# Kernel optimization log

Hardware: AMD Instinct MI355X
Metric: run time of the kernel (lower is better)

The kernel has to match this reference:

```python
import jax, jax.numpy as jnp
import numpy as np

LN_EPS = 1e-5


def _layer_norm(x, g, b):
    m = jnp.mean(x, axis=-1, keepdims=True)
    v = jnp.mean(jnp.square(x - m), axis=-1, keepdims=True)
    return (x - m) * jax.lax.rsqrt(v + LN_EPS) * g + b


def _transition(x, g, bln, w_sw, w_ss, w_sig, b_sig, w_scale, residual):
    # TransitionBlock, eval mode (dropout = identity)
    x_in = x
    x = _layer_norm(x, g, bln)
    b = jax.nn.silu(x @ w_sw.T) * (x @ w_ss.T)
    y = jax.nn.sigmoid(x @ w_sig.T + b_sig) * (b @ w_scale.T)
    return x_in + y if residual else y


def setup_inputs() -> dict:
    N, E = 1000000, 100000
    F_DIM, A_DIM, H_DIM, HEADS = 64, 128, 256, 4
    D_IN = F_DIM + A_DIM
    key = jax.random.key(0)
    ks = jax.random.split(key, 16)
    s = 0.02
    inp = {
        'v_equivariant': jax.random.normal(ks[0], (N, 3), jnp.float32),
        'v_atom_features': jax.random.normal(ks[1], (N, A_DIM), jnp.float32),
        'edge_group_idx': jnp.sort(jax.random.randint(ks[2], (N,), 0, E)).astype(jnp.int32),
        'num_edges': E,
        'fourier_w': jax.random.normal(ks[3], (F_DIM,), jnp.float32),
        'fourier_b': jax.random.normal(ks[4], (F_DIM,), jnp.float32),
        # TransitionBlock 1 (input 192 -> 256, no residual)
        'tb1_ln_g': jnp.ones((D_IN,), jnp.float32),
        'tb1_ln_b': jnp.zeros((D_IN,), jnp.float32),
        'tb1_w_sw': jax.random.normal(ks[5], (H_DIM, D_IN), jnp.float32) * s,
        'tb1_w_ss': jax.random.normal(ks[6], (H_DIM, D_IN), jnp.float32) * s,
        'tb1_w_sig': jax.random.normal(ks[7], (H_DIM, D_IN), jnp.float32) * s,
        'tb1_b_sig': jnp.full((H_DIM,), -2.0, jnp.float32),
        'tb1_w_scale': jax.random.normal(ks[8], (H_DIM, H_DIM), jnp.float32) * s,
        # TransitionBlock 2 (256 -> 256, residual)
        'tb2_ln_g': jnp.ones((H_DIM,), jnp.float32),
        'tb2_ln_b': jnp.zeros((H_DIM,), jnp.float32),
        'tb2_w_sw': jax.random.normal(ks[9], (H_DIM, H_DIM), jnp.float32) * s,
        'tb2_w_ss': jax.random.normal(ks[10], (H_DIM, H_DIM), jnp.float32) * s,
        'tb2_w_sig': jax.random.normal(ks[11], (H_DIM, H_DIM), jnp.float32) * s,
        'tb2_b_sig': jnp.full((H_DIM,), -2.0, jnp.float32),
        'tb2_w_scale': jax.random.normal(ks[12], (H_DIM, H_DIM), jnp.float32) * s,
        # final linear 256 -> num_heads
        'out_w': jax.random.normal(ks[13], (HEADS, H_DIM), jnp.float32) * s,
        'out_b': jnp.zeros((HEADS,), jnp.float32),
    }
    return inp


def reference(v_equivariant, v_atom_features, edge_group_idx, num_edges,
              fourier_w, fourier_b,
              tb1_ln_g, tb1_ln_b, tb1_w_sw, tb1_w_ss, tb1_w_sig, tb1_b_sig, tb1_w_scale,
              tb2_ln_g, tb2_ln_b, tb2_w_sw, tb2_w_ss, tb2_w_sig, tb2_b_sig, tb2_w_scale,
              out_w, out_b):
    # Fourier embedding of vector norms: [N] -> [N, F_DIM]
    v_norms = jnp.linalg.norm(v_equivariant, axis=-1)
    f_dist = jnp.cos(2.0 * jnp.pi * (v_norms[..., None] * fourier_w + fourier_b))
    x = jnp.concatenate([f_dist, v_atom_features], axis=-1)  # [N, 192]
    x = _transition(x, tb1_ln_g, tb1_ln_b, tb1_w_sw, tb1_w_ss, tb1_w_sig, tb1_b_sig, tb1_w_scale, residual=False)
    x = _transition(x, tb2_ln_g, tb2_ln_b, tb2_w_sw, tb2_w_ss, tb2_w_sig, tb2_b_sig, tb2_w_scale, residual=True)
    scores = x @ out_w.T + out_b  # [N, H]
    # scatter_softmax over edge groups (per head)
    smax = jax.ops.segment_max(scores, edge_group_idx, num_segments=num_edges)
    e = jnp.exp(scores - smax[edge_group_idx])
    ssum = jax.ops.segment_sum(e, edge_group_idx, num_segments=num_edges)
    alphas = e / ssum[edge_group_idx]  # [N, H]
    # weighted scatter-sum pooling of 3-vectors per head
    v_weighted = v_equivariant[:, None, :] * alphas[..., None]  # [N, H, 3]
    v_pooled = jax.ops.segment_sum(v_weighted, edge_group_idx, num_segments=num_edges)
    return v_pooled.reshape(num_edges, -1)  # [E, H*3]
```

## Files before the change

### kernel.cpp

```cpp
#include <hip/hip_runtime.h>
#include <math.h>

#define DIN   192
#define HD    256
#define ROWS  64
#define THREADS 512
#define LSTR  256

typedef __bf16 bf16_t;
typedef bf16_t bf16x8 __attribute__((ext_vector_type(8)));
typedef float  f32x16 __attribute__((ext_vector_type(16)));

static __device__ __forceinline__ f32x16 mfma32(bf16x8 a, bf16x8 b, f32x16 c) {
  return __builtin_amdgcn_mfma_f32_32x32x16_bf16(a, b, c, 0, 0, 0);
}
static __device__ __forceinline__ unsigned short f2bfu(float f) {
  bf16_t h = (bf16_t)f; unsigned short u; __builtin_memcpy(&u, &h, 2); return u;
}
static __device__ __forceinline__ float bfu2f(unsigned short u) {
  unsigned x = ((unsigned)u) << 16; float f; __builtin_memcpy(&f, &x, 4); return f;
}
static __device__ __forceinline__ unsigned pk2(float a, float b) {
  return (unsigned)f2bfu(a) | ((unsigned)f2bfu(b) << 16);
}
static __device__ __forceinline__ float lo16(unsigned u) { return bfu2f((unsigned short)(u & 0xffff)); }
static __device__ __forceinline__ float hi16(unsigned u) { return bfu2f((unsigned short)(u >> 16)); }
static __device__ __forceinline__ float sigm(float x) {
  return __builtin_amdgcn_rcpf(1.f + __expf(-x));
}
static __device__ __forceinline__ int lidx(int row, int col) {
  return row * LSTR + (col ^ ((row & 7) << 3));
}
static __device__ __forceinline__ int crow(int r, int kg) {
  return (r & 3) + 8 * (r >> 2) + 4 * kg;
}

#define OFF_WSW1 0
#define OFF_WSS1 49152
#define OFF_WSG1 98304
#define OFF_WSC1 147456
#define OFF_WSW2 212992
#define OFF_WSS2 278528
#define OFF_WSG2 344064
#define OFF_WSC2 409600
#define OFF_WOUT 475136
#define NGRP_REORD 59392
#define NGRP_ALL   60416

__global__ void iab_wconv_kernel(const float* __restrict__ a0, const float* __restrict__ a1,
                                 const float* __restrict__ a2, const float* __restrict__ a3,
                                 const float* __restrict__ a4, const float* __restrict__ a5,
                                 const float* __restrict__ a6, const float* __restrict__ a7,
                                 const float* __restrict__ a8, unsigned short* __restrict__ out)
{
  const int i = blockIdx.x * 256 + threadIdx.x;
  if (i >= NGRP_ALL) return;
  if (i >= NGRP_REORD) {
    const int g  = i - NGRP_REORD;
    const int ks = g >> 6;
    const int ln = g & 63;
    const int col = ln & 31;
    const int kg  = ln >> 5;
    #pragma unroll
    for (int j = 0; j < 8; ++j) {
      const float vv = (col < 4) ? a8[col * 256 + ks * 16 + kg * 8 + j] : 0.f;
      out[OFF_WOUT + (size_t)g * 8 + j] = f2bfu(vv);
    }
    return;
  }
  const float* src; int off, Kd, g;
  if      (i < 6144)  { src = a0; off = OFF_WSW1; Kd = 192; g = i; }
  else if (i < 12288) { src = a1; off = OFF_WSS1; Kd = 192; g = i - 6144; }
  else if (i < 18432) { src = a2; off = OFF_WSG1; Kd = 192; g = i - 12288; }
  else if (i < 26624) { src = a3; off = OFF_WSC1; Kd = 256; g = i - 18432; }
  else if (i < 34816) { src = a4; off = OFF_WSW2; Kd = 256; g = i - 26624; }
  else if (i < 43008) { src = a5; off = OFF_WSS2; Kd = 256; g = i - 34816; }
  else if (i < 51200) { src = a6; off = OFF_WSG2; Kd = 256; g = i - 43008; }
  else                { src = a7; off = OFF_WSC2; Kd = 256; g = i - 51200; }
  const int KS   = Kd >> 4;
  const int tile = g / (KS * 64);
  const int rem  = g - tile * (KS * 64);
  const int ks   = rem >> 6;
  const int ln   = rem & 63;
  const float* sp = src + (size_t)(tile * 32 + (ln & 31)) * Kd + ks * 16 + (ln >> 5) * 8;
  #pragma unroll
  for (int j = 0; j < 8; ++j) out[off + (size_t)g * 8 + j] = f2bfu(sp[j]);
}

template<int KS>
static __device__ __forceinline__ void gemm2(const unsigned short* __restrict__ Wt,
                                             const unsigned short* __restrict__ sIn,
                                             int l31, int kg, int xr,
                                             f32x16& acc0, f32x16& acc1)
{
  #pragma unroll 4
  for (int ks = 0; ks < KS; ++ks) {
    const bf16x8 Wc = *(const bf16x8*)(Wt + ks * 512);
    const int col = (ks * 16 + kg * 8) ^ xr;
    const bf16x8 A0 = *(const bf16x8*)(sIn + l31 * LSTR + col);
    const bf16x8 A1 = *(const bf16x8*)(sIn + (l31 + 32) * LSTR + col);
    acc0 = mfma32(A0, Wc, acc0);
    acc1 = mfma32(A1, Wc, acc1);
  }
}

template<int KS>
static __device__ __forceinline__ void gemm2p(const unsigned short* __restrict__ Wa,
                                              const unsigned short* __restrict__ Wb,
                                              const unsigned short* __restrict__ sIn,
                                              int l31, int kg, int xr,
                                              f32x16& u0, f32x16& u1,
                                              f32x16& s0, f32x16& s1)
{
  #pragma unroll 2
  for (int ks = 0; ks < KS; ++ks) {
    const bf16x8 wa = *(const bf16x8*)(Wa + ks * 512);
    const bf16x8 wb = *(const bf16x8*)(Wb + ks * 512);
    const int col = (ks * 16 + kg * 8) ^ xr;
    const bf16x8 A0 = *(const bf16x8*)(sIn + l31 * LSTR + col);
    const bf16x8 A1 = *(const bf16x8*)(sIn + (l31 + 32) * LSTR + col);
    u0 = mfma32(A0, wa, u0);
    s0 = mfma32(A0, wb, s0);
    u1 = mfma32(A1, wa, u1);
    s1 = mfma32(A1, wb, s1);
  }
}

static __device__ __forceinline__ void storeSilu2(unsigned short* dst, const f32x16 u,
                                                  const f32x16 s, int mt, int kg, int ocol)
{
  #pragma unroll
  for (int i = 0; i < 16; ++i) {
    const float x = u[i];
    dst[lidx(mt * 32 + crow(i, kg), ocol)] = f2bfu(x * sigm(x) * s[i]);
  }
}

static __device__ __forceinline__ void storePk(unsigned short* dst, const unsigned* xp,
                                               int kg, int ocol)
{
  #pragma unroll
  for (int mt = 0; mt < 2; ++mt) {
    #pragma unroll
    for (int p = 0; p < 8; ++p) {
      const int r0 = 2 * p;
      const int row0 = mt * 32 + crow(r0, kg);
      const unsigned pk = xp[mt * 8 + p];
      dst[lidx(row0,     ocol)] = (unsigned short)(pk & 0xffff);
      dst[lidx(row0 + 1, ocol)] = (unsigned short)(pk >> 16);
    }
  }
}

__global__ __launch_bounds__(THREADS, 2)
void iab_rows_mfma(
    const float* __restrict__ v, const float* __restrict__ af,
    const float* __restrict__ fw, const float* __restrict__ fb,
    const float* __restrict__ ln1g, const float* __restrict__ ln1b,
    const float* __restrict__ bsig1,
    const float* __restrict__ ln2g, const float* __restrict__ ln2b,
    const float* __restrict__ bsig2,
    const float* __restrict__ outb,
    const unsigned short* __restrict__ wc,
    float* __restrict__ scores, int N)
{
  __shared__ __align__(16) unsigned short sA[ROWS * LSTR];
  __shared__ __align__(16) unsigned short sB[ROWS * LSTR];

  const int t    = threadIdx.x;
  const int w    = t >> 6;
  const int lane = t & 63;
  const int l31  = lane & 31;
  const int kg   = lane >> 5;
  const int xr   = (lane & 7) << 3;
  const int ocol = w * 32 + l31;
  const int row0 = blockIdx.x * ROWS;

  const unsigned short* WtSW1 = wc + OFF_WSW1 + (w * 12 * 64 + lane) * 8;
  const unsigned short* WtSS1 = wc + OFF_WSS1 + (w * 12 * 64 + lane) * 8;
  const unsigned short* WtSG1 = wc + OFF_WSG1 + (w * 12 * 64 + lane) * 8;
  const unsigned short* WtSC1 = wc + OFF_WSC1 + (w * 16 * 64 + lane) * 8;
  const unsigned short* WtSW2 = wc + OFF_WSW2 + (w * 16 * 64 + lane) * 8;
  const unsigned short* WtSS2 = wc + OFF_WSS2 + (w * 16 * 64 + lane) * 8;
  const unsigned short* WtSG2 = wc + OFF_WSG2 + (w * 16 * 64 + lane) * 8;
  const unsigned short* WtSC2 = wc + OFF_WSC2 + (w * 16 * 64 + lane) * 8;

  {
    const float fwl = fw[lane], fbl = fb[lane];
    const float g1a = ln1g[lane], g1b = ln1g[lane + 64], g1c = ln1g[lane + 128];
    const float o1a = ln1b[lane], o1b = ln1b[lane + 64], o1c = ln1b[lane + 128];
    for (int rr = 0; rr < 8; ++rr) {
      const int r = w * 8 + rr;
      const int g = row0 + r;
      float e0 = 0.f, e1 = 0.f, e2 = 0.f;
      if (g < N) {
        const float vx = v[3 * (size_t)g + 0];
        const float vy = v[3 * (size_t)g + 1];
        const float vz = v[3 * (size_t)g + 2];
        const float nrm = sqrtf(vx * vx + vy * vy + vz * vz);
        e0 = __cosf(6.283185307179586f * (nrm * fwl + fbl));
        const float* a = af + (size_t)g * 128;
        e1 = a[lane];
        e2 = a[lane + 64];
      }
      float s  = e0 + e1 + e2;
      float sq = e0 * e0 + e1 * e1 + e2 * e2;
      #pragma unroll
      for (int o = 32; o >= 1; o >>= 1) {
        s  += __shfl_xor(s,  o);
        sq += __shfl_xor(sq, o);
      }
      const float mean = s * (1.f / 192.f);
      const float var  = fmaxf(sq * (1.f / 192.f) - mean * mean, 0.f);
      const float rstd = rsqrtf(var + 1e-5f);
      sA[lidx(r, lane)]       = f2bfu((e0 - mean) * rstd * g1a + o1a);
      sA[lidx(r, lane + 64)]  = f2bfu((e1 - mean) * rstd * g1b + o1b);
      sA[lidx(r, lane + 128)] = f2bfu((e2 - mean) * rstd * g1c + o1c);
    }
  }
  __syncthreads();

  unsigned x2p[16];

  {
    f32x16 u0{}, u1{}, s0{}, s1{};
    gemm2p<12>(WtSW1, WtSS1, sA, l31, kg, xr, u0, u1, s0, s1);
    storeSilu2(sB, u0, s0, 0, kg, ocol);
    storeSilu2(sB, u1, s1, 1, kg, ocol);
  }

  unsigned sgp[16];
  {
    f32x16 g0{}, g1{};
    gemm2<12>(WtSG1, sA, l31, kg, xr, g0, g1);
    const float bias = bsig1[ocol];
    #pragma unroll
    for (int p = 0; p < 8; ++p) {
      sgp[p]     = pk2(sigm(g0[2*p] + bias), sigm(g0[2*p+1] + bias));
      sgp[8 + p] = pk2(sigm(g1[2*p] + bias), sigm(g1[2*p+1] + bias));
    }
  }
  __syncthreads();

  {
    f32x16 c0{}, c1{};
    gemm2<16>(WtSC1, sB, l31, kg, xr, c0, c1);
    #pragma unroll
    for (int p = 0; p < 8; ++p) {
      x2p[p]     = pk2(lo16(sgp[p])   * c0[2*p], hi16(sgp[p])   * c0[2*p+1]);
      x2p[8 + p] = pk2(lo16(sgp[8+p]) * c1[2*p], hi16(sgp[8+p]) * c1[2*p+1]);
    }
    storePk(sA, x2p, kg, ocol);
  }
  __syncthreads();

  {
    float g2v[4], o2v[4];
    #pragma unroll
    for (int i = 0; i < 4; ++i) { g2v[i] = ln2g[lane + 64 * i]; o2v[i] = ln2b[lane + 64 * i]; }
    for (int rr = 0; rr < 8; ++rr) {
      const int r = w * 8 + rr;
      float e[4];
      #pragma unroll
      for (int i = 0; i < 4; ++i) e[i] = bfu2f(sA[lidx(r, lane + 64 * i)]);
      float s  = e[0] + e[1] + e[2] + e[3];
      float sq = e[0]*e[0] + e[1]*e[1] + e[2]*e[2] + e[3]*e[3];
      #pragma unroll
      for (int o = 32; o >= 1; o >>= 1) {
        s  += __shfl_xor(s,  o);
        sq += __shfl_xor(sq, o);
      }
      const float mean = s * (1.f / 256.f);
      const float var  = fmaxf(sq * (1.f / 256.f) - mean * mean, 0.f);
      const float rstd = rsqrtf(var + 1e-5f);
      #pragma unroll
      for (int i = 0; i < 4; ++i)
        sA[lidx(r, lane + 64 * i)] = f2bfu((e[i] - mean) * rstd * g2v[i] + o2v[i]);
    }
  }
  __syncthreads();

  {
    f32x16 u0{}, u1{}, s0{}, s1{};
    gemm2p<16>(WtSW2, WtSS2, sA, l31, kg, xr, u0, u1, s0, s1);
    storeSilu2(sB, u0, s0, 0, kg, ocol);
    storeSilu2(sB, u1, s1, 1, kg, ocol);
  }

  {
    f32x16 g0{}, g1{};
    gemm2<16>(WtSG2, sA, l31, kg, xr, g0, g1);
    const float bias = bsig2[ocol];
    #pragma unroll
    for (int p = 0; p < 8; ++p) {
      sgp[p]     = pk2(sigm(g0[2*p] + bias), sigm(g0[2*p+1] + bias));
      sgp[8 + p] = pk2(sigm(g1[2*p] + bias), sigm(g1[2*p+1] + bias));
    }
  }
  __syncthreads();

  {
    f32x16 c0{}, c1{};
    gemm2<16>(WtSC2, sB, l31, kg, xr, c0, c1);
    #pragma unroll
    for (int p = 0; p < 8; ++p) {
      x2p[p]     = pk2(lo16(x2p[p])   + lo16(sgp[p])   * c0[2*p],
                       hi16(x2p[p])   + hi16(sgp[p])   * c0[2*p+1]);
      x2p[8 + p] = pk2(lo16(x2p[8+p]) + lo16(sgp[8+p]) * c1[2*p],
                       hi16(x2p[8+p]) + hi16(sgp[8+p]) * c1[2*p+1]);
    }
    storePk(sA, x2p, kg, ocol);
  }
  __syncthreads();

  if (w < 2) {
    const unsigned short* WtF = wc + OFF_WOUT + (size_t)lane * 8;
    f32x16 c{};
    #pragma unroll 4
    for (int ks = 0; ks < 16; ++ks) {
      const bf16x8 wf = *(const bf16x8*)(WtF + ks * 512);
      const int col = (ks * 16 + kg * 8) ^ xr;
      const bf16x8 A = *(const bf16x8*)(sA + (w * 32 + l31) * LSTR + col);
      c = mfma32(A, wf, c);
    }
    if (l31 < 4) {
      const float bias = outb[l31];
      #pragma unroll
      for (int i = 0; i < 16; ++i) {
        const int g = row0 + w * 32 + crow(i, kg);
        if (g < N) scores[(size_t)g * 4 + l31] = c[i] + bias;
      }
    }
  }
}

__device__ __forceinline__ int iab_lower_bound(const int* __restrict__ a, int n, int key)
{
  int lo = 0, hi = n;
  while (lo < hi) {
    const int mid = (lo + hi) >> 1;
    if (a[mid] < key) lo = mid + 1; else hi = mid;
  }
  return lo;
}

__global__ __launch_bounds__(256)
void iab_segpool_kernel(const float* __restrict__ scores,
                        const float* __restrict__ v,
                        const int* __restrict__ gidx,
                        float* __restrict__ out, int N, int E)
{
  const int seg  = blockIdx.x * 4 + (threadIdx.x >> 6);
  const int lane = threadIdx.x & 63;
  if (seg >= E) return;

  const int lo = iab_lower_bound(gidx, N, seg);
  const int hi = iab_lower_bound(gidx, N, seg + 1);

  const int h  = lane & 3;
  const int ro = lane >> 2;

  float m = -INFINITY;
  for (int base = lo; base < hi; base += 16) {
    const int r = base + ro;
    if (r < hi) m = fmaxf(m, scores[(size_t)r * 4 + h]);
  }
  #pragma unroll
  for (int o = 4; o < 64; o <<= 1) m = fmaxf(m, __shfl_xor(m, o));

  float ssum = 0.f, w0 = 0.f, w1 = 0.f, w2 = 0.f;
  for (int base = lo; base < hi; base += 16) {
    const int r = base + ro;
    if (r < hi) {
      const float e = expf(scores[(size_t)r * 4 + h] - m);
      ssum += e;
      w0 += e * v[3 * (size_t)r + 0];
      w1 += e * v[3 * (size_t)r + 1];
      w2 += e * v[3 * (size_t)r + 2];
    }
  }
  #pragma unroll
  for (int o = 4; o < 64; o <<= 1) {
    ssum += __shfl_xor(ssum, o);
    w0   += __shfl_xor(w0, o);
    w1   += __shfl_xor(w1, o);
    w2   += __shfl_xor(w2, o);
  }

  if (ro == 0) {
    const float inv = (hi > lo) ? (1.f / ssum) : 0.f;
    out[(size_t)seg * 12 + h * 3 + 0] = w0 * inv;
    out[(size_t)seg * 12 + h * 3 + 1] = w1 * inv;
    out[(size_t)seg * 12 + h * 3 + 2] = w2 * inv;
  }
}

extern "C" void kernel_launch(void* const* d_in, const int* in_sizes, int n_in,
                              void* d_out, int out_size, void* d_ws, size_t ws_size,
                              hipStream_t stream)
{
  const float* v     = (const float*)d_in[0];
  const float* af    = (const float*)d_in[1];
  const int*   gidx  = (const int*)  d_in[2];
  const float* fw    = (const float*)d_in[4];
  const float* fb    = (const float*)d_in[5];
  const float* ln1g  = (const float*)d_in[6];
  const float* ln1b  = (const float*)d_in[7];
  const float* wsw1  = (const float*)d_in[8];
  const float* wss1  = (const float*)d_in[9];
  const float* wsig1 = (const float*)d_in[10];
  const float* bsig1 = (const float*)d_in[11];
  const float* wsc1  = (const float*)d_in[12];
  const float* ln2g  = (const float*)d_in[13];
  const float* ln2b  = (const float*)d_in[14];
  const float* wsw2  = (const float*)d_in[15];
  const float* wss2  = (const float*)d_in[16];
  const float* wsig2 = (const float*)d_in[17];
  const float* bsig2 = (const float*)d_in[18];
  const float* wsc2  = (const float*)d_in[19];
  const float* outw  = (const float*)d_in[20];
  const float* outb  = (const float*)d_in[21];

  const int N = in_sizes[0] / 3;
  const int E = out_size / 12;

  float* scores = (float*)d_ws;
  unsigned short* wcv = (unsigned short*)((char*)d_ws + (size_t)N * 4 * sizeof(float));

  hipLaunchKernelGGL(iab_wconv_kernel, dim3((NGRP_ALL + 255) / 256), dim3(256), 0, stream,
                     wsw1, wss1, wsig1, wsc1, wsw2, wss2, wsig2, wsc2, outw, wcv);

  hipLaunchKernelGGL(iab_rows_mfma, dim3((N + ROWS - 1) / ROWS), dim3(THREADS), 0, stream,
                     v, af, fw, fb, ln1g, ln1b, bsig1, ln2g, ln2b, bsig2, outb,
                     wcv, scores, N);

  hipLaunchKernelGGL(iab_segpool_kernel, dim3((E + 3) / 4), dim3(256), 0, stream,
                     scores, v, gidx, (float*)d_out, N, E);
}
```

Measured before the change: 1.948 ms.

## Halve row tile to 32 rows with 4 waves each covering two column tiles

The fused MLP kernel now processes 32 rows per block with 256 threads instead of 64 rows with 512 threads. Each wave computes two 32-column output tiles over a single 32-row tile rather than one column tile over two row tiles. Shared memory per block halves and the occupancy hint rises to 5 blocks per SM. The layer norms are rewritten so 8 threads share a row and use vectorized 16-byte LDS and global accesses. The cost is that each weight fragment is reused across only 32 rows, so weight traffic from global or L2 per row doubles.

```diff
diff --git a/kernel.cpp b/kernel.cpp
--- a/kernel.cpp
+++ b/kernel.cpp
@@ -3,12 +3,13 @@
 
 #define DIN   192
 #define HD    256
-#define ROWS  64
-#define THREADS 512
+#define ROWS  32
+#define THREADS 256
 #define LSTR  256
 
 typedef __bf16 bf16_t;
 typedef bf16_t bf16x8 __attribute__((ext_vector_type(8)));
+typedef unsigned short u16x8 __attribute__((ext_vector_type(8)));
 typedef float  f32x16 __attribute__((ext_vector_type(16)));
 
 static __device__ __forceinline__ f32x16 mfma32(bf16x8 a, bf16x8 b, f32x16 c) {
@@ -88,71 +89,58 @@
 }
 
 template<int KS>
-static __device__ __forceinline__ void gemm2(const unsigned short* __restrict__ Wt,
+static __device__ __forceinline__ void gemm1(const unsigned short* __restrict__ Wt,
                                              const unsigned short* __restrict__ sIn,
-                                             int l31, int kg, int xr,
-                                             f32x16& acc0, f32x16& acc1)
+                                             int l31, int kg, int xr, f32x16& acc)
 {
   #pragma unroll 4
   for (int ks = 0; ks < KS; ++ks) {
     const bf16x8 Wc = *(const bf16x8*)(Wt + ks * 512);
-    const int col = (ks * 16 + kg * 8) ^ xr;
-    const bf16x8 A0 = *(const bf16x8*)(sIn + l31 * LSTR + col);
-    const bf16x8 A1 = *(const bf16x8*)(sIn + (l31 + 32) * LSTR + col);
-    acc0 = mfma32(A0, Wc, acc0);
-    acc1 = mfma32(A1, Wc, acc1);
+    const bf16x8 A  = *(const bf16x8*)(sIn + l31 * LSTR + (((ks * 16) + kg * 8) ^ xr));
+    acc = mfma32(A, Wc, acc);
   }
 }
 
 template<int KS>
-static __device__ __forceinline__ void gemm2p(const unsigned short* __restrict__ Wa,
+static __device__ __forceinline__ void gemm1p(const unsigned short* __restrict__ Wa,
                                               const unsigned short* __restrict__ Wb,
                                               const unsigned short* __restrict__ sIn,
                                               int l31, int kg, int xr,
-                                              f32x16& u0, f32x16& u1,
-                                              f32x16& s0, f32x16& s1)
-{
-  #pragma unroll 2
+                                              f32x16& u, f32x16& s)
+{
+  #pragma unroll 4
   for (int ks = 0; ks < KS; ++ks) {
     const bf16x8 wa = *(const bf16x8*)(Wa + ks * 512);
     const bf16x8 wb = *(const bf16x8*)(Wb + ks * 512);
-    const int col = (ks * 16 + kg * 8) ^ xr;
-    const bf16x8 A0 = *(const bf16x8*)(sIn + l31 * LSTR + col);
-    const bf16x8 A1 = *(const bf16x8*)(sIn + (l31 + 32) * LSTR + col);
-    u0 = mfma32(A0, wa, u0);
-    s0 = mfma32(A0, wb, s0);
-    u1 = mfma32(A1, wa, u1);
-    s1 = mfma32(A1, wb, s1);
-  }
-}
-
-static __device__ __forceinline__ void storeSilu2(unsigned short* dst, const f32x16 u,
-                                                  const f32x16 s, int mt, int kg, int ocol)
+    const bf16x8 A  = *(const bf16x8*)(sIn + l31 * LSTR + (((ks * 16) + kg * 8) ^ xr));
+    u = mfma32(A, wa, u);
+    s = mfma32(A, wb, s);
+  }
+}
+
+static __device__ __forceinline__ void storeSilu1(unsigned short* dst, const f32x16 u,
+                                                  const f32x16 s, int kg, int ocol)
 {
   #pragma unroll
   for (int i = 0; i < 16; ++i) {
     const float x = u[i];
-    dst[lidx(mt * 32 + crow(i, kg), ocol)] = f2bfu(x * sigm(x) * s[i]);
-  }
-}
-
-static __device__ __forceinline__ void storePk(unsigned short* dst, const unsigned* xp,
-                                               int kg, int ocol)
-{
-  #pragma unroll
-  for (int mt = 0; mt < 2; ++mt) {
-    #pragma unroll
-    for (int p = 0; p < 8; ++p) {
-      const int r0 = 2 * p;
-      const int row0 = mt * 32 + crow(r0, kg);
-      const unsigned pk = xp[mt * 8 + p];
-      dst[lidx(row0,     ocol)] = (unsigned short)(pk & 0xffff);
-      dst[lidx(row0 + 1, ocol)] = (unsigned short)(pk >> 16);
-    }
-  }
-}
-
-__global__ __launch_bounds__(THREADS, 2)
+    dst[lidx(crow(i, kg), ocol)] = f2bfu(x * sigm(x) * s[i]);
+  }
+}
+
+static __device__ __forceinline__ void storePk1(unsigned short* dst, const unsigned* xp,
+                                                int kg, int ocol)
+{
+  #pragma unroll
+  for (int p = 0; p < 8; ++p) {
+    const int row0 = crow(2 * p, kg);
+    const unsigned pk = xp[p];
+    dst[lidx(row0,     ocol)] = (unsigned short)(pk & 0xffff);
+    dst[lidx(row0 + 1, ocol)] = (unsigned short)(pk >> 16);
+  }
+}
+
+__global__ __launch_bounds__(THREADS, 5)
 void iab_rows_mfma(
     const float* __restrict__ v, const float* __restrict__ af,
     const float* __restrict__ fw, const float* __restrict__ fb,
@@ -173,161 +161,220 @@
   const int l31  = lane & 31;
   const int kg   = lane >> 5;
   const int xr   = (lane & 7) << 3;
-  const int ocol = w * 32 + l31;
   const int row0 = blockIdx.x * ROWS;
 
-  const unsigned short* WtSW1 = wc + OFF_WSW1 + (w * 12 * 64 + lane) * 8;
-  const unsigned short* WtSS1 = wc + OFF_WSS1 + (w * 12 * 64 + lane) * 8;
-  const unsigned short* WtSG1 = wc + OFF_WSG1 + (w * 12 * 64 + lane) * 8;
-  const unsigned short* WtSC1 = wc + OFF_WSC1 + (w * 16 * 64 + lane) * 8;
-  const unsigned short* WtSW2 = wc + OFF_WSW2 + (w * 16 * 64 + lane) * 8;
-  const unsigned short* WtSS2 = wc + OFF_WSS2 + (w * 16 * 64 + lane) * 8;
-  const unsigned short* WtSG2 = wc + OFF_WSG2 + (w * 16 * 64 + lane) * 8;
-  const unsigned short* WtSC2 = wc + OFF_WSC2 + (w * 16 * 64 + lane) * 8;
-
   {
-    const float fwl = fw[lane], fbl = fb[lane];
-    const float g1a = ln1g[lane], g1b = ln1g[lane + 64], g1c = ln1g[lane + 128];
-    const float o1a = ln1b[lane], o1b = ln1b[lane + 64], o1c = ln1b[lane + 128];
-    for (int rr = 0; rr < 8; ++rr) {
-      const int r = w * 8 + rr;
-      const int g = row0 + r;
-      float e0 = 0.f, e1 = 0.f, e2 = 0.f;
-      if (g < N) {
-        const float vx = v[3 * (size_t)g + 0];
-        const float vy = v[3 * (size_t)g + 1];
-        const float vz = v[3 * (size_t)g + 2];
-        const float nrm = sqrtf(vx * vx + vy * vy + vz * vz);
-        e0 = __cosf(6.283185307179586f * (nrm * fwl + fbl));
-        const float* a = af + (size_t)g * 128;
-        e1 = a[lane];
-        e2 = a[lane + 64];
-      }
-      float s  = e0 + e1 + e2;
-      float sq = e0 * e0 + e1 * e1 + e2 * e2;
+    const int r   = t >> 3;
+    const int sub = t & 7;
+    const int g   = row0 + r;
+    const int xrr = (r & 7) << 3;
+    float vx = 0.f, vy = 0.f, vz = 0.f;
+    if (g < N) {
+      vx = v[3 * (size_t)g + 0];
+      vy = v[3 * (size_t)g + 1];
+      vz = v[3 * (size_t)g + 2];
+    }
+    const float nrm = sqrtf(vx * vx + vy * vy + vz * vz);
+    float e[24];
+    {
+      const float4 fwa = *(const float4*)(fw + sub * 8);
+      const float4 fwb = *(const float4*)(fw + sub * 8 + 4);
+      const float4 fba = *(const float4*)(fb + sub * 8);
+      const float4 fbb = *(const float4*)(fb + sub * 8 + 4);
+      e[0] = __cosf(6.283185307179586f * (nrm * fwa.x + fba.x));
+      e[1] = __cosf(6.283185307179586f * (nrm * fwa.y + fba.y));
+      e[2] = __cosf(6.283185307179586f * (nrm * fwa.z + fba.z));
+      e[3] = __cosf(6.283185307179586f * (nrm * fwa.w + fba.w));
+      e[4] = __cosf(6.283185307179586f * (nrm * fwb.x + fbb.x));
+      e[5] = __cosf(6.283185307179586f * (nrm * fwb.y + fbb.y));
+      e[6] = __cosf(6.283185307179586f * (nrm * fwb.z + fbb.z));
+      e[7] = __cosf(6.283185307179586f * (nrm * fwb.w + fbb.w));
+    }
+    if (g < N) {
+      const float* ap = af + (size_t)g * 128 + sub * 8;
+      const float4 a0 = *(const float4*)(ap);
+      const float4 a1 = *(const float4*)(ap + 4);
+      const float4 a2 = *(const float4*)(ap + 64);
+      const float4 a3 = *(const float4*)(ap + 68);
+      e[8]  = a0.x; e[9]  = a0.y; e[10] = a0.z; e[11] = a0.w;
+      e[12] = a1.x; e[13] = a1.y; e[14] = a1.z; e[15] = a1.w;
+      e[16] = a2.x; e[17] = a2.y; e[18] = a2.z; e[19] = a2.w;
+      e[20] = a3.x; e[21] = a3.y; e[22] = a3.z; e[23] = a3.w;
+    } else {
       #pragma unroll
-      for (int o = 32; o >= 1; o >>= 1) {
-        s  += __shfl_xor(s,  o);
-        sq += __shfl_xor(sq, o);
-      }
-      const float mean = s * (1.f / 192.f);
-      const float var  = fmaxf(sq * (1.f / 192.f) - mean * mean, 0.f);
-      const float rstd = rsqrtf(var + 1e-5f);
-      sA[lidx(r, lane)]       = f2bfu((e0 - mean) * rstd * g1a + o1a);
-      sA[lidx(r, lane + 64)]  = f2bfu((e1 - mean) * rstd * g1b + o1b);
-      sA[lidx(r, lane + 128)] = f2bfu((e2 - mean) * rstd * g1c + o1c);
+      for (int j = 8; j < 24; ++j) e[j] = 0.f;
+    }
+    float s = 0.f, sq = 0.f;
+    #pragma unroll
+    for (int j = 0; j < 24; ++j) { s += e[j]; sq += e[j] * e[j]; }
+    #pragma unroll
+    for (int o = 1; o < 8; o <<= 1) {
+      s  += __shfl_xor(s,  o);
+      sq += __shfl_xor(sq, o);
+    }
+    const float mean = s * (1.f / 192.f);
+    const float var  = fmaxf(sq * (1.f / 192.f) - mean * mean, 0.f);
+    const float rstd = rsqrtf(var + 1e-5f);
+    #pragma unroll
+    for (int ch = 0; ch < 3; ++ch) {
+      const int base = ch * 64 + sub * 8;
+      const float4 ga = *(const float4*)(ln1g + base);
+      const float4 gb = *(const float4*)(ln1g + base + 4);
+      const float4 oa = *(const float4*)(ln1b + base);
+      const float4 ob = *(const float4*)(ln1b + base + 4);
+      u16x8 p;
+      p[0] = f2bfu((e[ch*8+0] - mean) * rstd * ga.x + oa.x);
+      p[1] = f2bfu((e[ch*8+1] - mean) * rstd * ga.y + oa.y);
+      p[2] = f2bfu((e[ch*8+2] - mean) * rstd * ga.z + oa.z);
+      p[3] = f2bfu((e[ch*8+3] - mean) * rstd * ga.w + oa.w);
+      p[4] = f2bfu((e[ch*8+4] - mean) * rstd * gb.x + ob.x);
+      p[5] = f2bfu((e[ch*8+5] - mean) * rstd * gb.y + ob.y);
+      p[6] = f2bfu((e[ch*8+6] - mean) * rstd * gb.z + ob.z);
+      p[7] = f2bfu((e[ch*8+7] - mean) * rstd * gb.w + ob.w);
+      *(u16x8*)(sA + r * LSTR + (base ^ xrr)) = p;
     }
   }
   __syncthreads();
 
   unsigned x2p[16];
+  unsigned sgp[16];
+
+  #pragma unroll
+  for (int c = 0; c < 2; ++c) {
+    const int ocol = w * 64 + c * 32 + l31;
+    const int T = w * 2 + c;
+    f32x16 u{}, s{};
+    gemm1p<12>(wc + OFF_WSW1 + T * 12 * 512 + lane * 8,
+               wc + OFF_WSS1 + T * 12 * 512 + lane * 8, sA, l31, kg, xr, u, s);
+    storeSilu1(sB, u, s, kg, ocol);
+  }
+
+  #pragma unroll
+  for (int c = 0; c < 2; ++c) {
+    const int ocol = w * 64 + c * 32 + l31;
+    const int T = w * 2 + c;
+    f32x16 gacc{};
+    gemm1<12>(wc + OFF_WSG1 + T * 12 * 512 + lane * 8, sA, l31, kg, xr, gacc);
+    const float bias = bsig1[ocol];
+    #pragma unroll
+    for (int p = 0; p < 8; ++p)
+      sgp[c * 8 + p] = pk2(sigm(gacc[2*p] + bias), sigm(gacc[2*p+1] + bias));
+  }
+  __syncthreads();
+
+  #pragma unroll
+  for (int c = 0; c < 2; ++c) {
+    const int ocol = w * 64 + c * 32 + l31;
+    const int T = w * 2 + c;
+    f32x16 cacc{};
+    gemm1<16>(wc + OFF_WSC1 + T * 16 * 512 + lane * 8, sB, l31, kg, xr, cacc);
+    #pragma unroll
+    for (int p = 0; p < 8; ++p)
+      x2p[c * 8 + p] = pk2(lo16(sgp[c*8+p]) * cacc[2*p],
+                           hi16(sgp[c*8+p]) * cacc[2*p+1]);
+    storePk1(sA, x2p + c * 8, kg, ocol);
+  }
+  __syncthreads();
 
   {
-    f32x16 u0{}, u1{}, s0{}, s1{};
-    gemm2p<12>(WtSW1, WtSS1, sA, l31, kg, xr, u0, u1, s0, s1);
-    storeSilu2(sB, u0, s0, 0, kg, ocol);
-    storeSilu2(sB, u1, s1, 1, kg, ocol);
-  }
-
-  unsigned sgp[16];
-  {
-    f32x16 g0{}, g1{};
-    gemm2<12>(WtSG1, sA, l31, kg, xr, g0, g1);
-    const float bias = bsig1[ocol];
-    #pragma unroll
-    for (int p = 0; p < 8; ++p) {
-      sgp[p]     = pk2(sigm(g0[2*p] + bias), sigm(g0[2*p+1] + bias));
-      sgp[8 + p] = pk2(sigm(g1[2*p] + bias), sigm(g1[2*p+1] + bias));
-    }
-  }
-  __syncthreads();
-
-  {
-    f32x16 c0{}, c1{};
-    gemm2<16>(WtSC1, sB, l31, kg, xr, c0, c1);
-    #pragma unroll
-    for (int p = 0; p < 8; ++p) {
-      x2p[p]     = pk2(lo16(sgp[p])   * c0[2*p], hi16(sgp[p])   * c0[2*p+1]);
-      x2p[8 + p] = pk2(lo16(sgp[8+p]) * c1[2*p], hi16(sgp[8+p]) * c1[2*p+1]);
-    }
-    storePk(sA, x2p, kg, ocol);
-  }
-  __syncthreads();
-
-  {
-    float g2v[4], o2v[4];
-    #pragma unroll
-    for (int i = 0; i < 4; ++i) { g2v[i] = ln2g[lane + 64 * i]; o2v[i] = ln2b[lane + 64 * i]; }
-    for (int rr = 0; rr < 8; ++rr) {
-      const int r = w * 8 + rr;
-      float e[4];
-      #pragma unroll
-      for (int i = 0; i < 4; ++i) e[i] = bfu2f(sA[lidx(r, lane + 64 * i)]);
-      float s  = e[0] + e[1] + e[2] + e[3];
-      float sq = e[0]*e[0] + e[1]*e[1] + e[2]*e[2] + e[3]*e[3];
-      #pragma unroll
-      for (int o = 32; o >= 1; o >>= 1) {
-        s  += __shfl_xor(s,  o);
-        sq += __shfl_xor(sq, o);
-      }
-      const float mean = s * (1.f / 256.f);
-      const float var  = fmaxf(sq * (1.f / 256.f) - mean * mean, 0.f);
-      const float rstd = rsqrtf(var + 1e-5f);
-      #pragma unroll
-      for (int i = 0; i < 4; ++i)
-        sA[lidx(r, lane + 64 * i)] = f2bfu((e[i] - mean) * rstd * g2v[i] + o2v[i]);
-    }
-  }
-  __syncthreads();
-
-  {
-    f32x16 u0{}, u1{}, s0{}, s1{};
-    gemm2p<16>(WtSW2, WtSS2, sA, l31, kg, xr, u0, u1, s0, s1);
-    storeSilu2(sB, u0, s0, 0, kg, ocol);
-    storeSilu2(sB, u1, s1, 1, kg, ocol);
-  }
-
-  {
-    f32x16 g0{}, g1{};
-    gemm2<16>(WtSG2, sA, l31, kg, xr, g0, g1);
+    const int r   = t >> 3;
+    const int sub = t & 7;
+    const int xrr = (r & 7) << 3;
+    u16x8 rv0 = *(const u16x8*)(sA + r * LSTR + ((sub * 32 +  0) ^ xrr));
+    u16x8 rv1 = *(const u16x8*)(sA + r * LSTR + ((sub * 32 +  8) ^ xrr));
+    u16x8 rv2 = *(const u16x8*)(sA + r * LSTR + ((sub * 32 + 16) ^ xrr));
+    u16x8 rv3 = *(const u16x8*)(sA + r * LSTR + ((sub * 32 + 24) ^ xrr));
+    float e[32];
+    #pragma unroll
+    for (int j = 0; j < 8; ++j) {
+      e[j]      = bfu2f(rv0[j]);
+      e[8 + j]  = bfu2f(rv1[j]);
+      e[16 + j] = bfu2f(rv2[j]);
+      e[24 + j] = bfu2f(rv3[j]);
+    }
+    float s = 0.f, sq = 0.f;
+    #pragma unroll
+    for (int j = 0; j < 32; ++j) { s += e[j]; sq += e[j] * e[j]; }
+    #pragma unroll
+    for (int o = 1; o < 8; o <<= 1) {
+      s  += __shfl_xor(s,  o);
+      sq += __shfl_xor(sq, o);
+    }
+    const float mean = s * (1.f / 256.f);
+    const float var  = fmaxf(sq * (1.f / 256.f) - mean * mean, 0.f);
+    const float rstd = rsqrtf(var + 1e-5f);
+    #pragma unroll
+    for (int c = 0; c < 4; ++c) {
+      const int base = sub * 32 + c * 8;
+      const float4 ga = *(const float4*)(ln2g + base);
+      const float4 gb = *(const float4*)(ln2g + base + 4);
+      const float4 oa = *(const float4*)(ln2b + base);
+      const float4 ob = *(const float4*)(ln2b + base + 4);
+      u16x8 p;
+      p[0] = f2bfu((e[c*8+0] - mean) * rstd * ga.x + oa.x);
+      p[1] = f2bfu((e[c*8+1] - mean) * rstd * ga.y + oa.y);
+      p[2] = f2bfu((e[c*8+2] - mean) * rstd * ga.z + oa.z);
+      p[3] = f2bfu((e[c*8+3] - mean) * rstd * ga.w + oa.w);
+      p[4] = f2bfu((e[c*8+4] - mean) * rstd * gb.x + ob.x);
+      p[5] = f2bfu((e[c*8+5] - mean) * rstd * gb.y + ob.y);
+      p[6] = f2bfu((e[c*8+6] - mean) * rstd * gb.z + ob.z);
+      p[7] = f2bfu((e[c*8+7] - mean) * rstd * gb.w + ob.w);
+      *(u16x8*)(sA + r * LSTR + (base ^ xrr)) = p;
+    }
+  }
+  __syncthreads();
+
+  #pragma unroll
+  for (int c = 0; c < 2; ++c) {
+    const int ocol = w * 64 + c * 32 + l31;
+    const int T = w * 2 + c;
+    f32x16 u{}, s{};
+    gemm1p<16>(wc + OFF_WSW2 + T * 16 * 512 + lane * 8,
+               wc + OFF_WSS2 + T * 16 * 512 + lane * 8, sA, l31, kg, xr, u, s);
+    storeSilu1(sB, u, s, kg, ocol);
+  }
+
+  #pragma unroll
+  for (int c = 0; c < 2; ++c) {
+    const int ocol = w * 64 + c * 32 + l31;
+    const int T = w * 2 + c;
+    f32x16 gacc{};
+    gemm1<16>(wc + OFF_WSG2 + T * 16 * 512 + lane * 8, sA, l31, kg, xr, gacc);
     const float bias = bsig2[ocol];
     #pragma unroll
-    for (int p = 0; p < 8; ++p) {
-      sgp[p]     = pk2(sigm(g0[2*p] + bias), sigm(g0[2*p+1] + bias));
-      sgp[8 + p] = pk2(sigm(g1[2*p] + bias), sigm(g1[2*p+1] + bias));
-    }
-  }
-  __syncthreads();
-
-  {
-    f32x16 c0{}, c1{};
-    gemm2<16>(WtSC2, sB, l31, kg, xr, c0, c1);
-    #pragma unroll
-    for (int p = 0; p < 8; ++p) {
-      x2p[p]     = pk2(lo16(x2p[p])   + lo16(sgp[p])   * c0[2*p],
-                       hi16(x2p[p])   + hi16(sgp[p])   * c0[2*p+1]);
-      x2p[8 + p] = pk2(lo16(x2p[8+p]) + lo16(sgp[8+p]) * c1[2*p],
-                       hi16(x2p[8+p]) + hi16(sgp[8+p]) * c1[2*p+1]);
-    }
-    storePk(sA, x2p, kg, ocol);
-  }
-  __syncthreads();
-
-  if (w < 2) {
+    for (int p = 0; p < 8; ++p)
+      sgp[c * 8 + p] = pk2(sigm(gacc[2*p] + bias), sigm(gacc[2*p+1] + bias));
+  }
+  __syncthreads();
+
+  #pragma unroll
+  for (int c = 0; c < 2; ++c) {
+    const int ocol = w * 64 + c * 32 + l31;
+    const int T = w * 2 + c;
+    f32x16 cacc{};
+    gemm1<16>(wc + OFF_WSC2 + T * 16 * 512 + lane * 8, sB, l31, kg, xr, cacc);
+    #pragma unroll
+    for (int p = 0; p < 8; ++p)
+      x2p[c * 8 + p] = pk2(lo16(x2p[c*8+p]) + lo16(sgp[c*8+p]) * cacc[2*p],
+                           hi16(x2p[c*8+p]) + hi16(sgp[c*8+p]) * cacc[2*p+1]);
+    storePk1(sA, x2p + c * 8, kg, ocol);
+  }
+  __syncthreads();
+
+  if (w == 0) {
     const unsigned short* WtF = wc + OFF_WOUT + (size_t)lane * 8;
     f32x16 c{};
     #pragma unroll 4
     for (int ks = 0; ks < 16; ++ks) {
       const bf16x8 wf = *(const bf16x8*)(WtF + ks * 512);
-      const int col = (ks * 16 + kg * 8) ^ xr;
-      const bf16x8 A = *(const bf16x8*)(sA + (w * 32 + l31) * LSTR + col);
+      const bf16x8 A  = *(const bf16x8*)(sA + l31 * LSTR + (((ks * 16) + kg * 8) ^ xr));
       c = mfma32(A, wf, c);
     }
     if (l31 < 4) {
       const float bias = outb[l31];
       #pragma unroll
       for (int i = 0; i < 16; ++i) {
-        const int g = row0 + w * 32 + crow(i, kg);
+        const int g = row0 + crow(i, kg);
         if (g < N) scores[(size_t)g * 4 + l31] = c[i] + bias;
       }
     }
```

Result: slower. 2.604 ms (+33.7%).
